# Optimization experiments

Measured on AMD Instinct MI355X. Metric: run time of the kernel, lower is better.

## Reference

```python
import jax, jax.numpy as jnp
import numpy as np

RATE = 0.999  # moving_average_rate
EPS_NORM = 1e-12
EPS_CNT = 1e-6


def l2norm(v, axis=-1):
    # matches torch F.normalize(dim=axis) with default eps
    n = jnp.sqrt(jnp.sum(v * v, axis=axis, keepdims=True))
    return v / jnp.maximum(n, EPS_NORM)


def setup_inputs() -> dict:
    key = jax.random.key(0)
    ks = jax.random.split(key, 7)
    b, c, h, w, k = 8, 256, 64, 64, 2048
    x = jax.random.normal(ks[0], (b, c, h, w), dtype=jnp.float32)
    y = jax.random.uniform(ks[1], (b, 4, h, w), dtype=jnp.float32)
    feat_w = jax.random.normal(ks[2], (k, c + 4), dtype=jnp.float32) * 0.02
    w1 = jax.random.normal(ks[3], (c + 4, c), dtype=jnp.float32) * 0.02
    b1 = jnp.zeros((c,), dtype=jnp.float32)
    w2 = jax.random.normal(ks[4], (c, c), dtype=jnp.float32) * 0.02
    b2 = jnp.zeros((c,), dtype=jnp.float32)
    return {"x": x, "y": y, "feat_w": feat_w, "w1": w1, "b1": b1, "w2": w2, "b2": b2}


def reference(x, y, feat_w, w1, b1, w2, b2):
    b, c, h, w = x.shape
    k = feat_w.shape[0]
    # flatten spatial: (n, c) with n = b*h*w
    x_flat = jnp.transpose(x, (0, 2, 3, 1)).reshape(-1, c)
    y_flat = jnp.transpose(y, (0, 2, 3, 1)).reshape(-1, 4)

    # cosine-similarity scores against codebook features (no grad in original)
    xn = l2norm(x_flat)                       # (n, c)
    mn = l2norm(feat_w[:, :-4])               # (k, c)
    score = xn @ mn.T                         # (n, k)

    # top1 EMA codebook update
    xy = jnp.concatenate([x_flat, y_flat], axis=1)          # (n, c+4)
    ind = jnp.argmax(score, axis=1)                          # (n,)
    counts = jax.ops.segment_sum(jnp.ones_like(ind, jnp.float32), ind, num_segments=k)  # (k,)
    sums = jax.ops.segment_sum(xy, ind, num_segments=k)      # (k, c+4)
    embed_mean = sums / (counts[:, None] + EPS_CNT)          # (k, c+4)
    new_w = feat_w * RATE + embed_mean * (1.0 - RATE)        # (k, c+4)

    # softmax attention over (updated) normalized codebook
    p = jax.nn.softmax(score, axis=1)                        # (n, k)
    out = p @ l2norm(new_w)                                  # (n, c+4)

    # MLP: Linear -> GELU -> Linear (drop=0)
    out = jax.nn.gelu(out @ w1 + b1) @ w2 + b2               # (n, c)
    return jnp.transpose(out.reshape(b, h, w, c), (0, 3, 1, 2))
```

## Files before the change

kernel.cpp:

```cpp
#include <hip/hip_runtime.h>
#include <cstdint>
#include <cstddef>


typedef short v8s __attribute__((ext_vector_type(8)));
typedef float v4f __attribute__((ext_vector_type(4)));

__device__ __forceinline__ unsigned short f2b(float f) {
  unsigned u = __float_as_uint(f);
  u = (u + 0x7FFFu + ((u >> 16) & 1u)) >> 16;
  return (unsigned short)u;
}
__device__ __forceinline__ float b2f(short s) {
  return __uint_as_float((unsigned)(unsigned short)s << 16);
}
__device__ __forceinline__ float gelu_t(float x) {
  float x3 = x * x * x;
  return 0.5f * x * (1.0f + tanhf(0.7978845608028654f * (x + 0.044715f * x3)));
}
__device__ __forceinline__ unsigned int mono(float f) {
  unsigned u = __float_as_uint(f);
  return (u & 0x80000000u) ? ~u : (u | 0x80000000u);
}

__global__ void transpose_norm_kernel(const float* __restrict__ x, short* __restrict__ xn,
                                      float* __restrict__ norms) {
  __shared__ float tile[32 * 257];
  __shared__ float part[8][32];
  __shared__ float invn[32];
  int t = threadIdx.x, bx = blockIdx.x;
  int b = bx >> 7, st = bx & 127;
  int s0 = st * 32;
  int sl = t & 31, cp = t >> 5;
  const float* xb = x + (size_t)b * 256 * 4096 + s0 + sl;
  float ss = 0.f;
#pragma unroll 4
  for (int i = 0; i < 32; ++i) {
    int c = cp * 32 + i;
    float v = xb[(size_t)c * 4096];
    tile[sl * 257 + c] = v;
    ss += v * v;
  }
  part[cp][sl] = ss;
  __syncthreads();
  if (t < 32) {
    float tot = 0.f;
#pragma unroll
    for (int p = 0; p < 8; ++p) tot += part[p][t];
    float nrm = fmaxf(sqrtf(tot), 1e-12f);
    invn[t] = 1.0f / nrm;
    norms[(size_t)b * 4096 + s0 + t] = nrm;
  }
  __syncthreads();
  size_t obase = ((size_t)b * 4096 + s0) * 256 + t;
  for (int s = 0; s < 32; ++s)
    xn[obase + (size_t)s * 256] = (short)f2b(tile[s * 257 + t] * invn[s]);
}

__global__ void cbnorm_kernel(const float* __restrict__ fw, short* __restrict__ mn) {
  int t = threadIdx.x;
  int wv = t >> 6, l = t & 63;
  int r = blockIdx.x * 4 + wv;
  const float* row = fw + (size_t)r * 260;
  float v[4]; float ss = 0.f;
#pragma unroll
  for (int p = 0; p < 4; ++p) { v[p] = row[l + p * 64]; ss += v[p] * v[p]; }
#pragma unroll
  for (int m = 1; m < 64; m <<= 1) ss += __shfl_xor(ss, m, 64);
  float inv = 1.0f / fmaxf(sqrtf(ss), 1e-12f);
#pragma unroll
  for (int p = 0; p < 4; ++p) mn[(size_t)r * 256 + l + p * 64] = (short)f2b(v[p] * inv);
}

template <int KTOT, int LDA, int LDB>
__device__ __forceinline__ void gemm_core(const short* __restrict__ A, const short* __restrict__ B,
                                          int mt, int nt, int t, v4f acc[4][4],
                                          short* As, short* Bs) {
  const int l = t & 63, w = t >> 6;
  const int wm = w >> 1, wn = w & 1;
  const int lane16 = l & 15, q4 = l >> 4;
#pragma unroll
  for (int i = 0; i < 4; ++i)
#pragma unroll
    for (int j = 0; j < 4; ++j)
#pragma unroll
      for (int r = 0; r < 4; ++r) acc[i][j][r] = 0.0f;
  const short* Abase = A + (size_t)(mt * 128) * LDA;
  const short* Bbase = B + (size_t)(nt * 128) * LDB;
  for (int kk = 0; kk < KTOT; kk += 32) {
#pragma unroll
    for (int i = 0; i < 2; ++i) {
      int idx = t + i * 256;
      int row = idx >> 2, ce = (idx & 3) * 8;
      v8s va = *(const v8s*)(Abase + (size_t)row * LDA + kk + ce);
      v8s vb = *(const v8s*)(Bbase + (size_t)row * LDB + kk + ce);
      *(v8s*)&As[row * 40 + ce] = va;
      *(v8s*)&Bs[row * 40 + ce] = vb;
    }
    __syncthreads();
    v8s af[4], bf[4];
#pragma unroll
    for (int i = 0; i < 4; ++i) af[i] = *(v8s*)&As[(wm * 64 + i * 16 + lane16) * 40 + q4 * 8];
#pragma unroll
    for (int j = 0; j < 4; ++j) bf[j] = *(v8s*)&Bs[(wn * 64 + j * 16 + lane16) * 40 + q4 * 8];
#pragma unroll
    for (int i = 0; i < 4; ++i)
#pragma unroll
      for (int j = 0; j < 4; ++j)
        acc[i][j] = __builtin_amdgcn_mfma_f32_16x16x32_bf16(af[i], bf[j], acc[i][j], 0, 0, 0);
    __syncthreads();
  }
}

__global__ __launch_bounds__(256, 2) void gemm1_kernel(const short* __restrict__ A, const short* __restrict__ B,
                                                       short* __restrict__ Q,
                                                       unsigned long long* __restrict__ packed,
                                                       float* __restrict__ lrow) {
  __shared__ __align__(16) short As[128 * 40];
  __shared__ __align__(16) short Bs[128 * 40];
  int t = threadIdx.x, bx = blockIdx.x;
  int mt = bx >> 4, nt = bx & 15;
  v4f acc[4][4];
  gemm_core<256, 256, 256>(A, B, mt, nt, t, acc, As, Bs);
  int l = t & 63, w = t >> 6, wm = w >> 1, wn = w & 1, lane16 = l & 15, q4 = l >> 4;
  int rowbase = mt * 128 + wm * 64, colbase = nt * 128 + wn * 64;
#pragma unroll
  for (int i = 0; i < 4; ++i) {
#pragma unroll
    for (int r = 0; r < 4; ++r) {
      int row_g = rowbase + i * 16 + q4 * 4 + r;
      float qs = 0.f;
      unsigned long long best = 0ull;
#pragma unroll
      for (int j = 0; j < 4; ++j) {
        float s = acc[i][j][r];
        int col_g = colbase + j * 16 + lane16;
        float qv = expm1f(s);
        Q[(size_t)row_g * 2048 + col_g] = (short)f2b(qv);
        qs += qv;
        unsigned long long key = ((unsigned long long)mono(s) << 32) |
                                 (unsigned long long)(unsigned int)(~(unsigned)col_g);
        if (key > best) best = key;
      }
#pragma unroll
      for (int m = 1; m < 16; m <<= 1) {
        unsigned long long ob = __shfl_xor(best, m, 64);
        if (ob > best) best = ob;
        qs += __shfl_xor(qs, m, 64);
      }
      if (lane16 == 0) {
        atomicMax(&packed[row_g], best);
        atomicAdd(&lrow[row_g], qs);
      }
    }
  }
}

__global__ void ind_kernel(const unsigned long long* __restrict__ packed,
                           int* __restrict__ ind, float* __restrict__ cnt) {
  int i = blockIdx.x * 256 + threadIdx.x;
  unsigned int lowbits = (unsigned int)(packed[i] & 0xFFFFFFFFull);
  int id = (int)(~lowbits);
  ind[i] = id;
  atomicAdd(&cnt[id], 1.0f);
}

__global__ void scan_kernel(const float* __restrict__ cnt, int* __restrict__ offs,
                            int* __restrict__ cursor) {
  __shared__ int part[256];
  int t = threadIdx.x;
  int local[8]; int s = 0;
#pragma unroll
  for (int i = 0; i < 8; ++i) { local[i] = s; s += (int)cnt[t * 8 + i]; }
  part[t] = s;
  __syncthreads();
  for (int off = 1; off < 256; off <<= 1) {
    int v = (t >= off) ? part[t - off] : 0;
    __syncthreads();
    part[t] += v;
    __syncthreads();
  }
  int base = (t > 0) ? part[t - 1] : 0;
#pragma unroll
  for (int i = 0; i < 8; ++i) {
    int o = base + local[i];
    offs[t * 8 + i] = o;
    cursor[t * 8 + i] = o;
  }
  if (t == 255) offs[2048] = part[255];
}

__global__ void fill_kernel(const int* __restrict__ ind, int* __restrict__ cursor,
                            int* __restrict__ sorted) {
  int i = blockIdx.x * 256 + threadIdx.x;
  int id = ind[i];
  int pos = atomicAdd(&cursor[id], 1);
  sorted[pos] = i;
}

__global__ void segsum_kernel(const short* __restrict__ xn, const float* __restrict__ norms,
                              const float* __restrict__ y, const int* __restrict__ offs,
                              const int* __restrict__ sorted, float* __restrict__ sums) {
  int r = blockIdx.x, t = threadIdx.x;
  int beg = offs[r], end = offs[r + 1];
  float a0 = 0.f, a1 = 0.f;
  for (int j = beg; j < end; ++j) {
    int node = sorted[j];
    float nm = norms[node];
    a0 += b2f(xn[(size_t)node * 256 + t]) * nm;
    if (t < 4) {
      int b = node >> 12, s = node & 4095;
      a1 += y[(size_t)b * 16384 + t * 4096 + s];
    }
  }
  sums[(size_t)r * 260 + t] = a0;
  if (t < 4) sums[(size_t)r * 260 + 256 + t] = a1;
}

__global__ void neww_kernel(const float* __restrict__ fw, const float* __restrict__ sums,
                            const float* __restrict__ cnt, short* __restrict__ nwt,
                            float* __restrict__ colsum) {
  int r = blockIdx.x;
  int l = threadIdx.x;
  float cv = cnt[r] + 1e-6f;
  float vals[5]; float ss = 0.f;
#pragma unroll
  for (int p = 0; p < 5; ++p) {
    int c = l + p * 64;
    float v = 0.f;
    if (c < 260) {
      float m = sums[(size_t)r * 260 + c] / cv;
      v = fw[(size_t)r * 260 + c] * 0.999f + m * 0.001f;
    }
    vals[p] = v; ss += v * v;
  }
#pragma unroll
  for (int m = 1; m < 64; m <<= 1) ss += __shfl_xor(ss, m, 64);
  float inv = 1.0f / fmaxf(sqrtf(ss), 1e-12f);
#pragma unroll
  for (int p = 0; p < 5; ++p) {
    int c = l + p * 64;
    if (c < 260) {
      float v = vals[p] * inv;
      nwt[(size_t)c * 2048 + r] = (short)f2b(v);
      atomicAdd(&colsum[c], v);
    }
  }
}

__global__ void const_kernel(const float* __restrict__ colsum, const float* __restrict__ w1,
                             const float* __restrict__ b1, const float* __restrict__ w2,
                             const float* __restrict__ b2, float* __restrict__ c0,
                             float* __restrict__ zc, float* __restrict__ hc,
                             float* __restrict__ oc) {
  __shared__ float c0s[260], hcs[256];
  int t = threadIdx.x;
  for (int c = t; c < 260; c += 256) {
    float v = colsum[c] * (1.0f / 2048.0f);
    c0s[c] = v; c0[c] = v;
  }
  __syncthreads();
  float z = b1[t];
  for (int i = 0; i < 260; ++i) z = fmaf(c0s[i], w1[(size_t)i * 256 + t], z);
  float h = gelu_t(z);
  zc[t] = z; hc[t] = h; hcs[t] = h;
  __syncthreads();
  float o = b2[t];
  for (int i = 0; i < 256; ++i) o = fmaf(hcs[i], w2[(size_t)i * 256 + t], o);
  oc[t] = o;
}

__global__ void wtrans_kernel(const float* __restrict__ w1, const float* __restrict__ w2,
                              short* __restrict__ w1t, short* __restrict__ w2t) {
  int j = blockIdx.x;
  int t = threadIdx.x;
  if (j < 256) {
    for (int i = t; i < 288; i += 64)
      w1t[(size_t)j * 288 + i] = (short)f2b(i < 260 ? w1[(size_t)i * 256 + j] : 0.0f);
  } else {
    int jj = j - 256;
    for (int i = t; i < 256; i += 64)
      w2t[(size_t)jj * 256 + i] = (short)f2b(w2[(size_t)i * 256 + jj]);
  }
}

__global__ __launch_bounds__(256, 2) void gemm2_kernel(const short* __restrict__ A, const short* __restrict__ B,
                                                       const float* __restrict__ lrow,
                                                       const float* __restrict__ colsum,
                                                       const float* __restrict__ c0,
                                                       short* __restrict__ D) {
  __shared__ __align__(16) short As[128 * 40];
  __shared__ __align__(16) short Bs[128 * 40];
  int t = threadIdx.x, bx = blockIdx.x;
  int mt = bx / 3, nt = bx % 3;
  v4f acc[4][4];
  gemm_core<2048, 2048, 2048>(A, B, mt, nt, t, acc, As, Bs);
  int l = t & 63, w = t >> 6, wm = w >> 1, wn = w & 1, lane16 = l & 15, q4 = l >> 4;
  int rowbase = mt * 128 + wm * 64, colbase = nt * 128 + wn * 64;
#pragma unroll
  for (int i = 0; i < 4; ++i) {
#pragma unroll
    for (int r = 0; r < 4; ++r) {
      int row_g = rowbase + i * 16 + q4 * 4 + r;
      float linv = 1.0f / (2048.0f + lrow[row_g]);
#pragma unroll
      for (int j = 0; j < 4; ++j) {
        int col_g = colbase + j * 16 + lane16;
        if (col_g < 288) {
          float v = 0.0f;
          if (col_g < 260) {
            float attn = (colsum[col_g] + acc[i][j][r]) * linv;
            v = attn - c0[col_g];
          }
          D[(size_t)row_g * 288 + col_g] = (short)f2b(v);
        }
      }
    }
  }
}

__global__ __launch_bounds__(256, 2) void gemm3_kernel(const short* __restrict__ A, const short* __restrict__ B,
                                                       const float* __restrict__ zc,
                                                       const float* __restrict__ hc,
                                                       short* __restrict__ E) {
  __shared__ __align__(16) short As[128 * 40];
  __shared__ __align__(16) short Bs[128 * 40];
  int t = threadIdx.x, bx = blockIdx.x;
  int mt = bx >> 1, nt = bx & 1;
  v4f acc[4][4];
  gemm_core<288, 288, 288>(A, B, mt, nt, t, acc, As, Bs);
  int l = t & 63, w = t >> 6, wm = w >> 1, wn = w & 1, lane16 = l & 15, q4 = l >> 4;
  int rowbase = mt * 128 + wm * 64, colbase = nt * 128 + wn * 64;
#pragma unroll
  for (int i = 0; i < 4; ++i)
#pragma unroll
    for (int r = 0; r < 4; ++r) {
      int row_g = rowbase + i * 16 + q4 * 4 + r;
#pragma unroll
      for (int j = 0; j < 4; ++j) {
        int col_g = colbase + j * 16 + lane16;
        float z = zc[col_g] + acc[i][j][r];
        E[(size_t)row_g * 256 + col_g] = (short)f2b(gelu_t(z) - hc[col_g]);
      }
    }
}

__global__ __launch_bounds__(256, 2) void gemm4_kernel(const short* __restrict__ A, const short* __restrict__ B,
                                                       const float* __restrict__ oc,
                                                       float* __restrict__ T) {
  __shared__ __align__(16) short As[128 * 40];
  __shared__ __align__(16) short Bs[128 * 40];
  int t = threadIdx.x, bx = blockIdx.x;
  int mt = bx >> 1, nt = bx & 1;
  v4f acc[4][4];
  gemm_core<256, 256, 256>(A, B, mt, nt, t, acc, As, Bs);
  int l = t & 63, w = t >> 6, wm = w >> 1, wn = w & 1, lane16 = l & 15, q4 = l >> 4;
  int rowbase = mt * 128 + wm * 64, colbase = nt * 128 + wn * 64;
#pragma unroll
  for (int i = 0; i < 4; ++i)
#pragma unroll
    for (int r = 0; r < 4; ++r) {
      int row_g = rowbase + i * 16 + q4 * 4 + r;
#pragma unroll
      for (int j = 0; j < 4; ++j) {
        int col_g = colbase + j * 16 + lane16;
        T[(size_t)row_g * 256 + col_g] = oc[col_g] + acc[i][j][r];
      }
    }
}

__global__ void outtrans_kernel(const float* __restrict__ tmp, float* __restrict__ out) {
  __shared__ float tl[64 * 65];
  int bx = blockIdx.x;
  int ct = bx & 3, rt = bx >> 2;
  int r0 = rt * 64, c0 = ct * 64;
  int t = threadIdx.x;
  int tr = t >> 6, tc = t & 63;
#pragma unroll
  for (int i = 0; i < 16; ++i) {
    int rr = tr + i * 4;
    tl[rr * 65 + tc] = tmp[(size_t)(r0 + rr) * 256 + c0 + tc];
  }
  __syncthreads();
  int b = r0 >> 12, sb = r0 & 4095;
#pragma unroll
  for (int i = 0; i < 16; ++i) {
    int ccl = tr + i * 4;
    out[(size_t)b * 1048576 + (size_t)(c0 + ccl) * 4096 + sb + tc] = tl[tc * 65 + ccl];
  }
}

extern "C" void kernel_launch(void* const* d_in, const int* in_sizes, int n_in,
                              void* d_out, int out_size, void* d_ws, size_t ws_size,
                              hipStream_t stream) {
  const float* x  = (const float*)d_in[0];
  const float* y  = (const float*)d_in[1];
  const float* fw = (const float*)d_in[2];
  const float* w1 = (const float*)d_in[3];
  const float* b1 = (const float*)d_in[4];
  const float* w2 = (const float*)d_in[5];
  const float* b2 = (const float*)d_in[6];
  float* out = (float*)d_out;
  char* ws = (char*)d_ws;

  short* qbuf = (short*)(ws + 0);
  float* tmpo = (float*)(ws + 0);
  short* xn   = (short*)(ws + 134217728);
  short* ebuf = xn;
  short* mn   = (short*)(ws + 150994944);
  unsigned long long* packed = (unsigned long long*)(ws + 152043520);
  float* lrow = (float*)(ws + 152305664);
  int*   ind  = (int*)(ws + 152436736);
  float* cnt  = (float*)(ws + 152567808);
  float* sums = (float*)(ws + 152576000);
  short* nwt  = (short*)(ws + 154705920);
  float* colsum = (float*)(ws + 156278784);
  float* c0   = (float*)(ws + 156279936);
  float* zc   = (float*)(ws + 156281088);
  float* hc   = (float*)(ws + 156282112);
  float* oc   = (float*)(ws + 156283136);
  short* w1t  = (short*)(ws + 156284160);
  short* w2t  = (short*)(ws + 156431616);
  short* dbuf = (short*)(ws + 156562688);
  float* norms  = (float*)(ws + 156562688);
  int*   offs   = (int*)(ws + 156693760);
  int*   cursor = (int*)(ws + 156702464);
  int*   sorted = (int*)(ws + 156710656);
  if (ws_size < 175437056ull) return;

  hipMemsetAsync(packed, 0, 262144, stream);
  hipMemsetAsync(lrow,   0, 131072, stream);
  hipMemsetAsync(cnt,    0, 8192, stream);
  hipMemsetAsync(nwt,    0, 1572864, stream);
  hipMemsetAsync(colsum, 0, 1152, stream);

  transpose_norm_kernel<<<1024, 256, 0, stream>>>(x, xn, norms);
  cbnorm_kernel<<<512, 256, 0, stream>>>(fw, mn);
  gemm1_kernel<<<4096, 256, 0, stream>>>(xn, mn, qbuf, packed, lrow);
  ind_kernel<<<128, 256, 0, stream>>>(packed, ind, cnt);
  scan_kernel<<<1, 256, 0, stream>>>(cnt, offs, cursor);
  fill_kernel<<<128, 256, 0, stream>>>(ind, cursor, sorted);
  segsum_kernel<<<2048, 256, 0, stream>>>(xn, norms, y, offs, sorted, sums);
  neww_kernel<<<2048, 64, 0, stream>>>(fw, sums, cnt, nwt, colsum);
  const_kernel<<<1, 256, 0, stream>>>(colsum, w1, b1, w2, b2, c0, zc, hc, oc);
  wtrans_kernel<<<512, 64, 0, stream>>>(w1, w2, w1t, w2t);
  gemm2_kernel<<<768, 256, 0, stream>>>(qbuf, nwt, lrow, colsum, c0, dbuf);
  gemm3_kernel<<<512, 256, 0, stream>>>(dbuf, w1t, zc, hc, ebuf);
  gemm4_kernel<<<512, 256, 0, stream>>>(ebuf, w2t, oc, tmpo);
  outtrans_kernel<<<2048, 256, 0, stream>>>(tmpo, out);
}
```

Baseline: 460.9 us.

## Use direct global-to-LDS async loads in GEMM core and fast exp/GELU epilogues

The shared GEMM core now stages A and B tiles with global_load_lds instructions straight into unpadded 32-wide LDS rows, instead of loading into registers and storing to padded 40-wide rows. Separately, expm1f becomes __expf(s)-1 and the tanh GELU is rewritten as an exp/reciprocal form using fast intrinsics. The intent is to cut register traffic and VALU cost in the tile loads and epilogues. Dropping the padding can cause LDS bank conflicts on the fragment reads, there is no explicit wait on the async loads before the barrier, and the fast math slightly changes accuracy.

```diff
diff --git a/kernel.cpp b/kernel.cpp
--- a/kernel.cpp
+++ b/kernel.cpp
@@ -18,9 +18,19 @@
   float x3 = x * x * x;
   return 0.5f * x * (1.0f + tanhf(0.7978845608028654f * (x + 0.044715f * x3)));
 }
+__device__ __forceinline__ float gelu_fast(float x) {
+  float u = 0.7978845608028654f * (x + 0.044715f * x * x * x);
+  float tt = __expf(2.0f * u);
+  return x * tt * __builtin_amdgcn_rcpf(tt + 1.0f);
+}
 __device__ __forceinline__ unsigned int mono(float f) {
   unsigned u = __float_as_uint(f);
   return (u & 0x80000000u) ? ~u : (u | 0x80000000u);
+}
+__device__ __forceinline__ void async16(const short* g, short* l) {
+  __builtin_amdgcn_global_load_lds(
+      (const __attribute__((address_space(1))) unsigned int*)g,
+      (__attribute__((address_space(3))) unsigned int*)l, 16, 0, 0);
 }
 
 __global__ void transpose_norm_kernel(const float* __restrict__ x, short* __restrict__ xn,
@@ -85,24 +95,23 @@
     for (int j = 0; j < 4; ++j)
 #pragma unroll
       for (int r = 0; r < 4; ++r) acc[i][j][r] = 0.0f;
-  const short* Abase = A + (size_t)(mt * 128) * LDA;
-  const short* Bbase = B + (size_t)(nt * 128) * LDB;
+  const int srow = (w << 5) + (l >> 2);
+  const int scol = (l & 3) << 3;
+  const short* ga = A + (size_t)(mt * 128 + srow) * LDA + scol;
+  const short* gb = B + (size_t)(nt * 128 + srow) * LDB + scol;
+  short* la = As + (w << 5) * 32;
+  short* lb = Bs + (w << 5) * 32;
   for (int kk = 0; kk < KTOT; kk += 32) {
-#pragma unroll
-    for (int i = 0; i < 2; ++i) {
-      int idx = t + i * 256;
-      int row = idx >> 2, ce = (idx & 3) * 8;
-      v8s va = *(const v8s*)(Abase + (size_t)row * LDA + kk + ce);
-      v8s vb = *(const v8s*)(Bbase + (size_t)row * LDB + kk + ce);
-      *(v8s*)&As[row * 40 + ce] = va;
-      *(v8s*)&Bs[row * 40 + ce] = vb;
-    }
+    async16(ga + kk, la);
+    async16(ga + (size_t)16 * LDA + kk, la + 16 * 32);
+    async16(gb + kk, lb);
+    async16(gb + (size_t)16 * LDB + kk, lb + 16 * 32);
     __syncthreads();
     v8s af[4], bf[4];
 #pragma unroll
-    for (int i = 0; i < 4; ++i) af[i] = *(v8s*)&As[(wm * 64 + i * 16 + lane16) * 40 + q4 * 8];
-#pragma unroll
-    for (int j = 0; j < 4; ++j) bf[j] = *(v8s*)&Bs[(wn * 64 + j * 16 + lane16) * 40 + q4 * 8];
+    for (int i = 0; i < 4; ++i) af[i] = *(const v8s*)&As[(wm * 64 + i * 16 + lane16) * 32 + q4 * 8];
+#pragma unroll
+    for (int j = 0; j < 4; ++j) bf[j] = *(const v8s*)&Bs[(wn * 64 + j * 16 + lane16) * 32 + q4 * 8];
 #pragma unroll
     for (int i = 0; i < 4; ++i)
 #pragma unroll
@@ -116,8 +125,8 @@
                                                        short* __restrict__ Q,
                                                        unsigned long long* __restrict__ packed,
                                                        float* __restrict__ lrow) {
-  __shared__ __align__(16) short As[128 * 40];
-  __shared__ __align__(16) short Bs[128 * 40];
+  __shared__ __align__(16) short As[128 * 32];
+  __shared__ __align__(16) short Bs[128 * 32];
   int t = threadIdx.x, bx = blockIdx.x;
   int mt = bx >> 4, nt = bx & 15;
   v4f acc[4][4];
@@ -135,7 +144,7 @@
       for (int j = 0; j < 4; ++j) {
         float s = acc[i][j][r];
         int col_g = colbase + j * 16 + lane16;
-        float qv = expm1f(s);
+        float qv = __expf(s) - 1.0f;
         Q[(size_t)row_g * 2048 + col_g] = (short)f2b(qv);
         qs += qv;
         unsigned long long key = ((unsigned long long)mono(s) << 32) |
@@ -289,8 +298,8 @@
                                                        const float* __restrict__ colsum,
                                                        const float* __restrict__ c0,
                                                        short* __restrict__ D) {
-  __shared__ __align__(16) short As[128 * 40];
-  __shared__ __align__(16) short Bs[128 * 40];
+  __shared__ __align__(16) short As[128 * 32];
+  __shared__ __align__(16) short Bs[128 * 32];
   int t = threadIdx.x, bx = blockIdx.x;
   int mt = bx / 3, nt = bx % 3;
   v4f acc[4][4];
@@ -323,8 +332,8 @@
                                                        const float* __restrict__ zc,
                                                        const float* __restrict__ hc,
                                                        short* __restrict__ E) {
-  __shared__ __align__(16) short As[128 * 40];
-  __shared__ __align__(16) short Bs[128 * 40];
+  __shared__ __align__(16) short As[128 * 32];
+  __shared__ __align__(16) short Bs[128 * 32];
   int t = threadIdx.x, bx = blockIdx.x;
   int mt = bx >> 1, nt = bx & 1;
   v4f acc[4][4];
@@ -340,7 +349,7 @@
       for (int j = 0; j < 4; ++j) {
         int col_g = colbase + j * 16 + lane16;
         float z = zc[col_g] + acc[i][j][r];
-        E[(size_t)row_g * 256 + col_g] = (short)f2b(gelu_t(z) - hc[col_g]);
+        E[(size_t)row_g * 256 + col_g] = (short)f2b(gelu_fast(z) - hc[col_g]);
       }
     }
 }
@@ -348,8 +357,8 @@
 __global__ __launch_bounds__(256, 2) void gemm4_kernel(const short* __restrict__ A, const short* __restrict__ B,
                                                        const float* __restrict__ oc,
                                                        float* __restrict__ T) {
-  __shared__ __align__(16) short As[128 * 40];
-  __shared__ __align__(16) short Bs[128 * 40];
+  __shared__ __align__(16) short As[128 * 32];
+  __shared__ __align__(16) short Bs[128 * 32];
   int t = threadIdx.x, bx = blockIdx.x;
   int mt = bx >> 1, nt = bx & 1;
   v4f acc[4][4];
```

Result: faster. 440.4 us (-4.5%).
